# Kernel tuning notes

Measured on AMD Instinct MI355X. Metric: run time of the kernel, lower is better.

The kernel has to match this reference:

```python
import jax, jax.numpy as jnp
from jax import lax
import numpy as np

B, S, V, E, H = 256, 1024, 288, 100, 128


def setup_inputs() -> dict:
    key = jax.random.key(0)
    ks = jax.random.split(key, 16)
    d = {
        "text": jax.random.randint(ks[0], (B, S), 0, V, dtype=jnp.int32),
        "emb": jax.random.normal(ks[1], (V, E), jnp.float32) * 0.1,
        "fcW": jax.random.normal(ks[2], (V, H), jnp.float32) * 0.1,
        "fcb": jax.random.normal(ks[3], (V,), jnp.float32) * 0.1,
    }
    in_dims = [E, H, H]
    for l in range(3):
        kk = jax.random.split(ks[4 + l], 4)
        d[f"Wih{l}"] = jax.random.normal(kk[0], (4 * H, in_dims[l]), jnp.float32) * 0.1
        d[f"Whh{l}"] = jax.random.normal(kk[1], (4 * H, H), jnp.float32) * 0.1
        d[f"bih{l}"] = jax.random.normal(kk[2], (4 * H,), jnp.float32) * 0.1
        d[f"bhh{l}"] = jax.random.normal(kk[3], (4 * H,), jnp.float32) * 0.1
    return d


def _lstm_layer(x, Wih, Whh, bih, bhh):
    # x: [S, B, in]; PyTorch gate order i, f, g, o
    xg = jnp.einsum('sbe,ge->sbg', x, Wih) + (bih + bhh)  # precompute input proj [S,B,4H]
    Hh = Whh.shape[1]
    WhhT = Whh.T

    def step(carry, xg_t):
        h, c = carry
        g = xg_t + h @ WhhT
        i, f, gg, o = jnp.split(g, 4, axis=-1)
        c = jax.nn.sigmoid(f) * c + jax.nn.sigmoid(i) * jnp.tanh(gg)
        h = jax.nn.sigmoid(o) * jnp.tanh(c)
        return (h, c), h

    b = x.shape[1]
    init = (jnp.zeros((b, Hh), x.dtype), jnp.zeros((b, Hh), x.dtype))
    _, hs = lax.scan(step, init, xg)
    return hs  # [S, B, H]


def reference(text, emb, Wih0, Whh0, bih0, bhh0, Wih1, Whh1, bih1, bhh1,
              Wih2, Whh2, bih2, bhh2, fcW, fcb):
    # embedding (dropout is identity in eval mode)
    x = emb[text]                  # [B, S, E]
    x = jnp.transpose(x, (1, 0, 2))  # time-major [S, B, E]
    x = _lstm_layer(x, Wih0, Whh0, bih0, bhh0)
    x = _lstm_layer(x, Wih1, Whh1, bih1, bhh1)
    x = _lstm_layer(x, Wih2, Whh2, bih2, bhh2)
    # fc head; original returns prediction.transpose(0,1) -> [S, B, V]
    pred = jnp.einsum('sbh,vh->sbv', x, fcW) + fcb
    return pred
```

## Files before the change

kernel.cpp:

```cpp
#include <hip/hip_runtime.h>
#include <cstddef>
#include <cstdint>

#define BB 256
#define SS 1024
#define VV 288
#define EE 100
#define HH 128
#define G4 512
#define CH 16
#define NCH (SS / CH)

typedef _Float16 half8 __attribute__((ext_vector_type(8)));
typedef float f32x4 __attribute__((ext_vector_type(4)));

__device__ __forceinline__ float sig_f(float x) {
    return __builtin_amdgcn_rcpf(1.0f +
           __builtin_amdgcn_exp2f(-1.4426950408889634f * x));
}
__device__ __forceinline__ float tanh2_f(float x) {
    return 2.0f * __builtin_amdgcn_rcpf(1.0f +
           __builtin_amdgcn_exp2f(-2.8853900817779268f * x)) - 1.0f;
}

__global__ __launch_bounds__(512) void proj_kernel(
    const float* __restrict__ emb, const float* __restrict__ Wih0,
    const float* __restrict__ bih0, const float* __restrict__ bhh0,
    float* __restrict__ table)
{
    __shared__ float er[EE];
    const int v = blockIdx.x;
    const int j = threadIdx.x;
    for (int e = j; e < EE; e += 512) er[e] = emb[v * EE + e];
    __syncthreads();
    float acc = bih0[j] + bhh0[j];
    const float* wr = Wih0 + j * EE;
#pragma unroll 4
    for (int e = 0; e < EE; e++) acc = fmaf(er[e], wr[e], acc);
    table[v * G4 + j] = acc;
}

__global__ __launch_bounds__(256) void pack_fc(
    const float* __restrict__ W, _Float16* __restrict__ out)
{
    const int tid = blockIdx.x * 256 + threadIdx.x;
    const int e  = tid & 7;
    const int l  = (tid >> 3) & 63;
    const int f  = tid >> 9;
    const int kc = f & 3, nt = f >> 2;
    const int n = nt * 16 + (l & 15);
    const int k = kc * 32 + (l >> 4) * 8 + e;
    out[tid] = (_Float16)W[n * HH + k];
}

__global__ __launch_bounds__(512)
__attribute__((amdgpu_waves_per_eu(2, 2)))
void lstm_pipe(const int* __restrict__ text, const float* __restrict__ table,
               const float* Whh0f,
               const float* Wih1f, const float* Whh1f,
               const float* __restrict__ bih1, const float* __restrict__ bhh1,
               const float* Wih2f, const float* Whh2f,
               const float* __restrict__ bih2, const float* __restrict__ bhh2,
               _Float16* hX, _Float16* hY, int* prog)
{
    __shared__ int tokL[SS * 16];
    __shared__ _Float16 Hb[2][2048];
    const int tid = threadIdx.x;
    const int w = tid >> 6, l = tid & 63;
    const int layer = blockIdx.x >> 4;
    const int bt = blockIdx.x & 15;
    const int B0 = bt * 16;
    const int colD = l & 15, qd = l >> 4;
    const int gcol = w * 16 + colD;

    const float* WhhF = (layer == 0) ? Whh0f : ((layer == 1) ? Whh1f : Whh2f);
    const float* WihF = (layer == 2) ? Wih2f : Wih1f;
    const float* bihp = (layer == 2) ? bih2 : bih1;
    const float* bhhp = (layer == 2) ? bhh2 : bhh1;
    const _Float16* xin = (layer == 1) ? hX : hY;
    _Float16* hout = (layer == 1) ? hY : hX;
    int* prog_src = prog + (layer - 1) * 16 + bt;
    int* prog_my  = prog + layer * 16 + bt;

    half8 whh[4][4], wih[4][4];
#pragma unroll
    for (int gt = 0; gt < 4; gt++)
#pragma unroll
        for (int kc = 0; kc < 4; kc++) {
            const int n = gt * 128 + gcol;
            const int k0 = kc * 32 + qd * 8;
            const float4 a0 = *(const float4*)(WhhF + (size_t)n * HH + k0);
            const float4 a1 = *(const float4*)(WhhF + (size_t)n * HH + k0 + 4);
            half8 hf;
            hf[0] = (_Float16)a0.x; hf[1] = (_Float16)a0.y;
            hf[2] = (_Float16)a0.z; hf[3] = (_Float16)a0.w;
            hf[4] = (_Float16)a1.x; hf[5] = (_Float16)a1.y;
            hf[6] = (_Float16)a1.z; hf[7] = (_Float16)a1.w;
            whh[gt][kc] = hf;
            if (layer) {
                const float4 b0 = *(const float4*)(WihF + (size_t)n * HH + k0);
                const float4 b1 = *(const float4*)(WihF + (size_t)n * HH + k0 + 4);
                half8 hg;
                hg[0] = (_Float16)b0.x; hg[1] = (_Float16)b0.y;
                hg[2] = (_Float16)b0.z; hg[3] = (_Float16)b0.w;
                hg[4] = (_Float16)b1.x; hg[5] = (_Float16)b1.y;
                hg[6] = (_Float16)b1.z; hg[7] = (_Float16)b1.w;
                wih[gt][kc] = hg;
            }
        }
    f32x4 bias_frag[4];
#pragma unroll
    for (int gt = 0; gt < 4; gt++) {
        float b = 0.0f;
        if (layer) {
            const int g = gt * 128 + gcol;
            b = bihp[g] + bhhp[g];
        }
        bias_frag[gt] = (f32x4){b, b, b, b};
    }
    if (layer == 0) {
        for (int kk = 0; kk < 32; kk++) {
            const int lin = kk * 512 + tid;
            const int b = lin >> 10, t = lin & 1023;
            tokL[t * 16 + b] = text[(((size_t)B0 + b) << 10) | t];
        }
    }
    for (int i = tid; i < 2048; i += 512) Hb[0][i] = (_Float16)0.0f;
    f32x4 c_acc = {0.f, 0.f, 0.f, 0.f};

    int rd_idx[4], wr_idx[4];
#pragma unroll
    for (int kc = 0; kc < 4; kc++)
        rd_idx[kc] = (colD * 128 + kc * 32 + qd * 8) ^ ((colD & 7) << 3);
#pragma unroll
    for (int r = 0; r < 4; r++) {
        const int rr = 4 * qd + r;
        wr_idx[r] = (rr * 128 + gcol) ^ ((rr & 7) << 3);
    }
    __syncthreads();

    auto wait_src = [&](int target) {
        int v = __hip_atomic_load(prog_src, __ATOMIC_RELAXED,
                                  __HIP_MEMORY_SCOPE_AGENT);
        while (v < target) {
            __builtin_amdgcn_s_sleep(8);
            v = __hip_atomic_load(prog_src, __ATOMIC_RELAXED,
                                  __HIP_MEMORY_SCOPE_AGENT);
        }
        v = __hip_atomic_load(prog_src, __ATOMIC_ACQUIRE,
                              __HIP_MEMORY_SCOPE_AGENT);
        asm volatile("" :: "v"(v));
    };
    auto signal = [&](int c) {
        asm volatile("s_waitcnt vmcnt(0)" ::: "memory");
        __builtin_amdgcn_s_barrier();
        if (tid == 0) {
            __threadfence();
            __hip_atomic_store(prog_my, (c + 1) * CH, __ATOMIC_RELEASE,
                               __HIP_MEMORY_SCOPE_AGENT);
        }
    };
    auto finish = [&](f32x4 (&acc)[4], int T, int nxt) {
#pragma unroll
        for (int r = 0; r < 4; r++) {
            const float si = sig_f(acc[0][r]);
            const float sf = sig_f(acc[1][r]);
            const float tg = tanh2_f(acc[2][r]);
            const float so = sig_f(acc[3][r]);
            const float cc = fmaf(sf, c_acc[r], si * tg);
            c_acc[r] = cc;
            const float hv = so * tanh2_f(cc);
            const _Float16 hh = (_Float16)hv;
            Hb[nxt][wr_idx[r]] = hh;
            hout[(uint32_t)(T * BB + B0 + 4 * qd + r) * HH + gcol] = hh;
        }
        asm volatile("s_waitcnt lgkmcnt(0)" ::: "memory");
        __builtin_amdgcn_s_barrier();
    };

    if (layer == 0) {
        f32x4 xgA[4], xgB[4];
        {
            const int4 tk0 = *(const int4*)&tokL[4 * qd];
            const float* g0 = table + (size_t)tk0.x * G4 + gcol;
            const float* g1 = table + (size_t)tk0.y * G4 + gcol;
            const float* g2 = table + (size_t)tk0.z * G4 + gcol;
            const float* g3 = table + (size_t)tk0.w * G4 + gcol;
#pragma unroll
            for (int gt = 0; gt < 4; gt++) {
                xgA[gt][0] = g0[gt * 128];
                xgA[gt][1] = g1[gt * 128];
                xgA[gt][2] = g2[gt * 128];
                xgA[gt][3] = g3[gt * 128];
            }
        }
        auto step0 = [&](int T, int cur, f32x4 (&xgc)[4], f32x4 (&xgn)[4]) {
            half8 a_h[4];
#pragma unroll
            for (int kc = 0; kc < 4; kc++)
                a_h[kc] = *(const half8*)&Hb[cur][rd_idx[kc]];
            const int Tn = (T + 1 < SS) ? T + 1 : T;
            const int4 tkn = *(const int4*)&tokL[Tn * 16 + 4 * qd];
            f32x4 acc[4];
#pragma unroll
            for (int gt = 0; gt < 4; gt++) {
                acc[gt] = __builtin_amdgcn_mfma_f32_16x16x32_f16(
                    a_h[0], whh[gt][0], xgc[gt], 0, 0, 0);
#pragma unroll
                for (int kc = 1; kc < 4; kc++)
                    acc[gt] = __builtin_amdgcn_mfma_f32_16x16x32_f16(
                        a_h[kc], whh[gt][kc], acc[gt], 0, 0, 0);
            }
            {
                const float* g0 = table + (size_t)tkn.x * G4 + gcol;
                const float* g1 = table + (size_t)tkn.y * G4 + gcol;
                const float* g2 = table + (size_t)tkn.z * G4 + gcol;
                const float* g3 = table + (size_t)tkn.w * G4 + gcol;
#pragma unroll
                for (int gt = 0; gt < 4; gt++) {
                    xgn[gt][0] = g0[gt * 128];
                    xgn[gt][1] = g1[gt * 128];
                    xgn[gt][2] = g2[gt * 128];
                    xgn[gt][3] = g3[gt * 128];
                }
            }
            finish(acc, T, cur ^ 1);
        };
        for (int c = 0; c < NCH; c++) {
            for (int tt = 0; tt < CH; tt += 2) {
                step0(c * CH + tt,     0, xgA, xgB);
                step0(c * CH + tt + 1, 1, xgB, xgA);
            }
            signal(c);
        }
    } else {
        wait_src(2 * CH);
        const _Float16* xbase = xin + ((size_t)B0 + colD) * HH + qd * 8;
        half8 xA[4], xB[4];
#pragma unroll
        for (int kc = 0; kc < 4; kc++) {
            xA[kc] = *(const half8*)(xbase + (size_t)0 * BB * HH + kc * 32);
            xB[kc] = *(const half8*)(xbase + (size_t)1 * BB * HH + kc * 32);
        }
        auto stepK = [&](int T, int cur, half8 (&xcur)[4]) {
            half8 a_h[4];
#pragma unroll
            for (int kc = 0; kc < 4; kc++)
                a_h[kc] = *(const half8*)&Hb[cur][rd_idx[kc]];
            f32x4 acc[4];
#pragma unroll
            for (int gt = 0; gt < 4; gt++) {
                acc[gt] = __builtin_amdgcn_mfma_f32_16x16x32_f16(
                    xcur[0], wih[gt][0], bias_frag[gt], 0, 0, 0);
#pragma unroll
                for (int kc = 1; kc < 4; kc++)
                    acc[gt] = __builtin_amdgcn_mfma_f32_16x16x32_f16(
                        xcur[kc], wih[gt][kc], acc[gt], 0, 0, 0);
            }
            {
                const size_t tf =
                    (T + 2 < SS) ? (size_t)(T + 2) : (size_t)(SS - 1);
#pragma unroll
                for (int kc = 0; kc < 4; kc++)
                    xcur[kc] = *(const half8*)(xbase + tf * BB * HH + kc * 32);
            }
#pragma unroll
            for (int kc = 0; kc < 4; kc++)
#pragma unroll
                for (int gt = 0; gt < 4; gt++)
                    acc[gt] = __builtin_amdgcn_mfma_f32_16x16x32_f16(
                        a_h[kc], whh[gt][kc], acc[gt], 0, 0, 0);
            finish(acc, T, cur ^ 1);
        };
        for (int c = 0; c < NCH; c++) {
            if (c) {
                const int tgt = (c + 2) * CH;
                wait_src(tgt > SS ? SS : tgt);
            }
            for (int tt = 0; tt < CH; tt += 2) {
                stepK(c * CH + tt,     0, xA);
                stepK(c * CH + tt + 1, 1, xB);
            }
            if (layer == 1) signal(c);
        }
    }
}

__global__ __launch_bounds__(256) void fc_mfma(
    const _Float16* __restrict__ h2, const _Float16* __restrict__ pfcW,
    const float* __restrict__ fcb, float* __restrict__ out)
{
    const int tid = threadIdx.x, wv = tid >> 6, l = tid & 63;
    const int colD = l & 15, qd = l >> 4;
    const size_t m0 = (size_t)blockIdx.x * 64 + wv * 16;
    half8 a[4];
#pragma unroll
    for (int kc = 0; kc < 4; kc++)
        a[kc] = *(const half8*)(h2 + (m0 + colD) * HH + kc * 32 + qd * 8);
    float fcb_r[18];
#pragma unroll
    for (int nt = 0; nt < 18; nt++) fcb_r[nt] = fcb[nt * 16 + colD];
#pragma unroll
    for (int nt = 0; nt < 18; nt++) {
        f32x4 acc = {0.f, 0.f, 0.f, 0.f};
#pragma unroll
        for (int kc = 0; kc < 4; kc++) {
            const half8 b = *(const half8*)(pfcW + (((nt * 4 + kc) << 6) + l) * 8);
            acc = __builtin_amdgcn_mfma_f32_16x16x32_f16(a[kc], b, acc, 0, 0, 0);
        }
#pragma unroll
        for (int r = 0; r < 4; r++)
            out[(m0 + 4 * qd + r) * VV + nt * 16 + colD] = acc[r] + fcb_r[nt];
    }
}

extern "C" void kernel_launch(void* const* d_in, const int* in_sizes, int n_in,
                              void* d_out, int out_size, void* d_ws, size_t ws_size,
                              hipStream_t stream)
{
    (void)in_sizes; (void)n_in; (void)ws_size;
    const int*   text = (const int*)  d_in[0];
    const float* emb  = (const float*)d_in[1];
    const float* fcW  = (const float*)d_in[2];
    const float* fcb  = (const float*)d_in[3];
    const float* Wih0 = (const float*)d_in[4];
    const float* Whh0 = (const float*)d_in[5];
    const float* bih0 = (const float*)d_in[6];
    const float* bhh0 = (const float*)d_in[7];
    const float* Wih1 = (const float*)d_in[8];
    const float* Whh1 = (const float*)d_in[9];
    const float* bih1 = (const float*)d_in[10];
    const float* bhh1 = (const float*)d_in[11];
    const float* Wih2 = (const float*)d_in[12];
    const float* Whh2 = (const float*)d_in[13];
    const float* bih2 = (const float*)d_in[14];
    const float* bhh2 = (const float*)d_in[15];
    float* out = (float*)d_out;

    float* table = (float*)d_ws;
    _Float16* hX = (_Float16*)((char*)d_ws + 589824);
    _Float16* hY = hX + (size_t)SS * BB * HH;
    _Float16* pfcW = (_Float16*)d_ws;
    int* prog = ((int*)d_out) + ((size_t)out_size - 64);

    hipMemsetAsync(prog, 0, 64 * sizeof(int), stream);
    proj_kernel<<<VV, 512, 0, stream>>>(emb, Wih0, bih0, bhh0, table);
    lstm_pipe<<<48, 512, 0, stream>>>(text, table, Whh0,
                                      Wih1, Whh1, bih1, bhh1,
                                      Wih2, Whh2, bih2, bhh2,
                                      hX, hY, prog);
    pack_fc<<<144, 256, 0, stream>>>(fcW, pfcW);
    fc_mfma<<<4096, 256, 0, stream>>>(hX, pfcW, fcb, out);
}
```

Baseline: 1.727 ms.

## Shorten recurrent MFMA chain by splitting accumulators and precomputing next input projection

The 4-deep dependent MFMA chain for the recurrent h@Whh product is split into two independent 2-deep chains whose results are summed in the gate epilogue. For layers 1 and 2, the input projection for the next timestep is computed after the current recurrent MFMAs and carried in registers, so it sits off the critical path. The hout store address is also advanced incrementally instead of being recomputed each step. The cost is more live accumulator registers and a few extra adds per gate, which may reduce occupancy or cause spills.

Result: faster. 1.603 ms (-7.2%).

```diff
diff --git a/kernel.cpp b/kernel.cpp
--- a/kernel.cpp
+++ b/kernel.cpp
@@ -137,6 +137,7 @@
         const int rr = 4 * qd + r;
         wr_idx[r] = (rr * 128 + gcol) ^ ((rr & 7) << 3);
     }
+    _Float16* houtp = hout + ((size_t)B0 + 4 * qd) * HH + gcol;
     __syncthreads();
 
     auto wait_src = [&](int target) {
@@ -160,20 +161,25 @@
                                __HIP_MEMORY_SCOPE_AGENT);
         }
     };
-    auto finish = [&](f32x4 (&acc)[4], int T, int nxt) {
+    auto finish = [&](f32x4 (&p)[4], f32x4 (&q)[4], int nxt) {
 #pragma unroll
         for (int r = 0; r < 4; r++) {
-            const float si = sig_f(acc[0][r]);
-            const float sf = sig_f(acc[1][r]);
-            const float tg = tanh2_f(acc[2][r]);
-            const float so = sig_f(acc[3][r]);
+            const float gi = p[0][r] + q[0][r];
+            const float gf = p[1][r] + q[1][r];
+            const float gg = p[2][r] + q[2][r];
+            const float go = p[3][r] + q[3][r];
+            const float si = sig_f(gi);
+            const float sf = sig_f(gf);
+            const float tg = tanh2_f(gg);
+            const float so = sig_f(go);
             const float cc = fmaf(sf, c_acc[r], si * tg);
             c_acc[r] = cc;
             const float hv = so * tanh2_f(cc);
             const _Float16 hh = (_Float16)hv;
             Hb[nxt][wr_idx[r]] = hh;
-            hout[(uint32_t)(T * BB + B0 + 4 * qd + r) * HH + gcol] = hh;
-        }
+            houtp[r * HH] = hh;
+        }
+        houtp += BB * HH;
         asm volatile("s_waitcnt lgkmcnt(0)" ::: "memory");
         __builtin_amdgcn_s_barrier();
     };
@@ -201,15 +207,17 @@
                 a_h[kc] = *(const half8*)&Hb[cur][rd_idx[kc]];
             const int Tn = (T + 1 < SS) ? T + 1 : T;
             const int4 tkn = *(const int4*)&tokL[Tn * 16 + 4 * qd];
-            f32x4 acc[4];
+            f32x4 p[4], q[4];
 #pragma unroll
             for (int gt = 0; gt < 4; gt++) {
-                acc[gt] = __builtin_amdgcn_mfma_f32_16x16x32_f16(
+                f32x4 t = __builtin_amdgcn_mfma_f32_16x16x32_f16(
                     a_h[0], whh[gt][0], xgc[gt], 0, 0, 0);
-#pragma unroll
-                for (int kc = 1; kc < 4; kc++)
-                    acc[gt] = __builtin_amdgcn_mfma_f32_16x16x32_f16(
-                        a_h[kc], whh[gt][kc], acc[gt], 0, 0, 0);
+                p[gt] = __builtin_amdgcn_mfma_f32_16x16x32_f16(
+                    a_h[1], whh[gt][1], t, 0, 0, 0);
+                f32x4 u = __builtin_amdgcn_mfma_f32_16x16x32_f16(
+                    a_h[2], whh[gt][2], (f32x4){0.f, 0.f, 0.f, 0.f}, 0, 0, 0);
+                q[gt] = __builtin_amdgcn_mfma_f32_16x16x32_f16(
+                    a_h[3], whh[gt][3], u, 0, 0, 0);
             }
             {
                 const float* g0 = table + (size_t)tkn.x * G4 + gcol;
@@ -224,7 +232,7 @@
                     xgn[gt][3] = g3[gt * 128];
                 }
             }
-            finish(acc, T, cur ^ 1);
+            finish(p, q, cur ^ 1);
         };
         for (int c = 0; c < NCH; c++) {
             for (int tt = 0; tt < CH; tt += 2) {
@@ -236,26 +244,49 @@
     } else {
         wait_src(2 * CH);
         const _Float16* xbase = xin + ((size_t)B0 + colD) * HH + qd * 8;
-        half8 xA[4], xB[4];
-#pragma unroll
-        for (int kc = 0; kc < 4; kc++) {
-            xA[kc] = *(const half8*)(xbase + (size_t)0 * BB * HH + kc * 32);
-            xB[kc] = *(const half8*)(xbase + (size_t)1 * BB * HH + kc * 32);
-        }
-        auto stepK = [&](int T, int cur, half8 (&xcur)[4]) {
+        half8 xcur[4];
+        f32x4 accXA[4], accXB[4];
+#pragma unroll
+        for (int kc = 0; kc < 4; kc++)
+            xcur[kc] = *(const half8*)(xbase + (size_t)0 * BB * HH + kc * 32);
+#pragma unroll
+        for (int gt = 0; gt < 4; gt++) {
+            f32x4 t = bias_frag[gt];
+#pragma unroll
+            for (int kc = 0; kc < 4; kc++)
+                t = __builtin_amdgcn_mfma_f32_16x16x32_f16(
+                    xcur[kc], wih[gt][kc], t, 0, 0, 0);
+            accXA[gt] = t;
+        }
+#pragma unroll
+        for (int kc = 0; kc < 4; kc++)
+            xcur[kc] = *(const half8*)(xbase + (size_t)1 * BB * HH + kc * 32);
+
+        auto stepK = [&](int T, int cur, f32x4 (&accXc)[4], f32x4 (&accXn)[4]) {
             half8 a_h[4];
 #pragma unroll
             for (int kc = 0; kc < 4; kc++)
                 a_h[kc] = *(const half8*)&Hb[cur][rd_idx[kc]];
-            f32x4 acc[4];
+            f32x4 p[4], q[4];
 #pragma unroll
             for (int gt = 0; gt < 4; gt++) {
-                acc[gt] = __builtin_amdgcn_mfma_f32_16x16x32_f16(
-                    xcur[0], wih[gt][0], bias_frag[gt], 0, 0, 0);
-#pragma unroll
-                for (int kc = 1; kc < 4; kc++)
-                    acc[gt] = __builtin_amdgcn_mfma_f32_16x16x32_f16(
-                        xcur[kc], wih[gt][kc], acc[gt], 0, 0, 0);
+                f32x4 t = __builtin_amdgcn_mfma_f32_16x16x32_f16(
+                    a_h[0], whh[gt][0], accXc[gt], 0, 0, 0);
+                p[gt] = __builtin_amdgcn_mfma_f32_16x16x32_f16(
+                    a_h[1], whh[gt][1], t, 0, 0, 0);
+                f32x4 u = __builtin_amdgcn_mfma_f32_16x16x32_f16(
+                    a_h[2], whh[gt][2], (f32x4){0.f, 0.f, 0.f, 0.f}, 0, 0, 0);
+                q[gt] = __builtin_amdgcn_mfma_f32_16x16x32_f16(
+                    a_h[3], whh[gt][3], u, 0, 0, 0);
+            }
+#pragma unroll
+            for (int gt = 0; gt < 4; gt++) {
+                f32x4 t = bias_frag[gt];
+#pragma unroll
+                for (int kc = 0; kc < 4; kc++)
+                    t = __builtin_amdgcn_mfma_f32_16x16x32_f16(
+                        xcur[kc], wih[gt][kc], t, 0, 0, 0);
+                accXn[gt] = t;
             }
             {
                 const size_t tf =
@@ -264,13 +295,7 @@
                 for (int kc = 0; kc < 4; kc++)
                     xcur[kc] = *(const half8*)(xbase + tf * BB * HH + kc * 32);
             }
-#pragma unroll
-            for (int kc = 0; kc < 4; kc++)
-#pragma unroll
-                for (int gt = 0; gt < 4; gt++)
-                    acc[gt] = __builtin_amdgcn_mfma_f32_16x16x32_f16(
-                        a_h[kc], whh[gt][kc], acc[gt], 0, 0, 0);
-            finish(acc, T, cur ^ 1);
+            finish(p, q, cur ^ 1);
         };
         for (int c = 0; c < NCH; c++) {
             if (c) {
@@ -278,8 +303,8 @@
                 wait_src(tgt > SS ? SS : tgt);
             }
             for (int tt = 0; tt < CH; tt += 2) {
-                stepK(c * CH + tt,     0, xA);
-                stepK(c * CH + tt + 1, 1, xB);
+                stepK(c * CH + tt,     0, accXA, accXB);
+                stepK(c * CH + tt + 1, 1, accXB, accXA);
             }
             if (layer == 1) signal(c);
         }
```
